# Kernel optimization log

Hardware: AMD Instinct MI355X
Metric: run time of the kernel (lower is better)

Reference implementation:

```python
import jax, jax.numpy as jnp
import numpy as np
from jax import lax

NB_VERTICES = 2048  # init kwarg nb_vertices
N_POINTS = 524288


def setup_inputs() -> dict:
    key = jax.random.key(0)
    pos = jax.random.normal(key, (N_POINTS, 3), dtype=jnp.float32)
    return {"pos": pos}


def _fps_indices(pos, m):
    """Single-pass iterative farthest point sampling.
    pos: [N, 3] float. Returns int32 indices [m].
    Maintains a running min squared-distance buffer (classic FPS).
    """
    N = pos.shape[0]
    big = jnp.asarray(jnp.finfo(pos.dtype).max, pos.dtype)
    min_d = jnp.full((N,), big, dtype=pos.dtype)
    idxs = jnp.zeros((m,), dtype=jnp.int32)  # idxs[0] = 0 (deterministic start)

    def body(i, carry):
        min_d, idxs = carry
        last = jnp.take(pos, idxs[i - 1], axis=0)          # [3]
        d = jnp.sum((pos - last[None, :]) ** 2, axis=-1)    # [N]
        min_d = jnp.minimum(min_d, d)
        nxt = jnp.argmax(min_d).astype(jnp.int32)
        idxs = idxs.at[i].set(nxt)
        return (min_d, idxs)

    _, idxs = lax.fori_loop(1, m, body, (min_d, idxs))
    return idxs


@jax.jit
def _forward(pos):
    # ratio = nb_vertices / N  ->  fps returns ceil(N*ratio) = nb_vertices
    # indices in a single pass, so the original while-loop runs once.
    idxs = _fps_indices(pos, NB_VERTICES)
    return pos[idxs]  # [nb_vertices, 3]


def reference(pos):
    return _forward(pos)
```

## Files before the change

### kernel.cpp

```cpp
#include <hip/hip_runtime.h>
#include <float.h>


#define NPTS     524288
#define MOUT     2048
#define NBLK     64
#define NTHR     512
#define NWAVE    (NTHR / 64)
#define GTHREADS (NBLK * NTHR)
#define PPT      (NPTS / GTHREADS)
#define SLOT_STRIDE 8
#define MASK51   ((1ull << 51) - 1)


__global__ void __launch_bounds__(NTHR, 1) fps_kernel(
    const float* __restrict__ pos, float* __restrict__ out,
    unsigned long long* __restrict__ slots)
{
    const unsigned tid = threadIdx.x;
    const unsigned blk = blockIdx.x;
    const unsigned g   = blk * NTHR + tid;

    float X[PPT], Y[PPT], Z[PPT], D[PPT];
#pragma unroll
    for (int p = 0; p < PPT; ++p) {
        const unsigned idx = g + (unsigned)p * GTHREADS;
        X[p] = pos[3u * idx + 0];
        Y[p] = pos[3u * idx + 1];
        Z[p] = pos[3u * idx + 2];
        D[p] = FLT_MAX;
    }

    float px = pos[0], py = pos[1], pz = pos[2];
    if (g == 0) { out[0] = px; out[1] = py; out[2] = pz; }

    __shared__ unsigned long long sred[NWAVE];
    __shared__ float sx, sy, sz;

    for (int i = 1; i < MOUT; ++i) {
        float bv = -1.0f;
        unsigned bi = 0;
#pragma unroll
        for (int p = 0; p < PPT; ++p) {
            float dx = __fsub_rn(X[p], px);
            float dy = __fsub_rn(Y[p], py);
            float dz = __fsub_rn(Z[p], pz);
            float d  = __fadd_rn(__fadd_rn(__fmul_rn(dx, dx), __fmul_rn(dy, dy)),
                                 __fmul_rn(dz, dz));
            float m  = fminf(D[p], d);
            D[p] = m;
            if (m > bv) { bv = m; bi = g + (unsigned)p * GTHREADS; }
        }
        unsigned long long best =
            ((unsigned long long)__float_as_uint(bv) << 19) |
            (unsigned long long)((NPTS - 1u) - bi);

#pragma unroll
        for (int off = 32; off > 0; off >>= 1) {
            unsigned long long o = __shfl_down(best, off, 64);
            if (o > best) best = o;
        }
        if ((tid & 63u) == 0u) sred[tid >> 6] = best;
        __syncthreads();

        if (tid < 64u) {
            unsigned long long b2 = (tid < NWAVE) ? sred[tid] : 0ull;
#pragma unroll
            for (int off = NWAVE / 2; off > 0; off >>= 1) {
                unsigned long long o = __shfl_down(b2, off, 64);
                if (o > b2) b2 = o;
            }
            unsigned long long* buf = slots + (unsigned)(i & 1) * (NBLK * SLOT_STRIDE);
            if (tid == 0u) {
                __hip_atomic_store(&buf[blk * SLOT_STRIDE],
                                   ((unsigned long long)i << 51) | b2,
                                   __ATOMIC_RELAXED, __HIP_MEMORY_SCOPE_AGENT);
            }
            const unsigned long long tag = (unsigned long long)i;
            unsigned long long s;
            do {
                s = __hip_atomic_load(&buf[tid * SLOT_STRIDE],
                                      __ATOMIC_RELAXED, __HIP_MEMORY_SCOPE_AGENT);
                if ((s >> 51) == tag) break;
                __builtin_amdgcn_s_sleep(1);
            } while (true);
            unsigned long long v = s & MASK51;
#pragma unroll
            for (int off = 32; off > 0; off >>= 1) {
                unsigned long long o = __shfl_down(v, off, 64);
                if (o > v) v = o;
            }
            if (tid == 0u) {
                unsigned widx = (NPTS - 1u) - (unsigned)(v & 0x7FFFFull);
                float x = pos[3u * widx + 0];
                float y = pos[3u * widx + 1];
                float z = pos[3u * widx + 2];
                sx = x; sy = y; sz = z;
                if (blk == 0) {
                    out[3 * i + 0] = x; out[3 * i + 1] = y; out[3 * i + 2] = z;
                }
            }
        }
        __syncthreads();
        px = sx; py = sy; pz = sz;
    }
}

extern "C" void kernel_launch(void* const* d_in, const int* in_sizes, int n_in,
                              void* d_out, int out_size, void* d_ws, size_t ws_size,
                              hipStream_t stream) {
    const float* pos = (const float*)d_in[0];
    float* out = (float*)d_out;
    unsigned long long* slots = (unsigned long long*)d_ws;

    void* args[] = { (void*)&pos, (void*)&out, (void*)&slots };
    hipLaunchCooperativeKernel((void*)fps_kernel, dim3(NBLK), dim3(NTHR),
                               args, 0, stream);
}
```

Before: 5.265 ms.

## Use single-wave blocks to drop intra-block barriers in FPS reduction

Changes the grid to 512 blocks of one 64-thread wave each. This removes the shared-memory stage and both __syncthreads per iteration. Each wave publishes its argmax to a global slot, then every wave polls all 512 slots itself, reduces them, and has each lane prefetch its own candidate's coordinates before the final shuffle reduction. The aim is to cut barrier and serial-lane latency on the critical path of each of the 2048 iterations. The cost is more global polling traffic per iteration, and a cooperative launch of 512 blocks must all be co-resident.

Result: slower. 9.101 ms (+72.8%).

```diff
diff --git a/kernel.cpp b/kernel.cpp
--- a/kernel.cpp
+++ b/kernel.cpp
@@ -4,12 +4,11 @@
 
 #define NPTS     524288
 #define MOUT     2048
-#define NBLK     64
-#define NTHR     512
-#define NWAVE    (NTHR / 64)
+#define NBLK     512
+#define NTHR     64
 #define GTHREADS (NBLK * NTHR)
 #define PPT      (NPTS / GTHREADS)
-#define SLOT_STRIDE 8
+#define KPL      (NBLK / 64)
 #define MASK51   ((1ull << 51) - 1)
 
 
@@ -17,9 +16,9 @@
     const float* __restrict__ pos, float* __restrict__ out,
     unsigned long long* __restrict__ slots)
 {
-    const unsigned tid = threadIdx.x;
-    const unsigned blk = blockIdx.x;
-    const unsigned g   = blk * NTHR + tid;
+    const unsigned lane = threadIdx.x;
+    const unsigned blk  = blockIdx.x;
+    const unsigned g    = blk * NTHR + lane;
 
     float X[PPT], Y[PPT], Z[PPT], D[PPT];
 #pragma unroll
@@ -33,9 +32,6 @@
 
     float px = pos[0], py = pos[1], pz = pos[2];
     if (g == 0) { out[0] = px; out[1] = py; out[2] = pz; }
-
-    __shared__ unsigned long long sred[NWAVE];
-    __shared__ float sx, sy, sz;
 
     for (int i = 1; i < MOUT; ++i) {
         float bv = -1.0f;
@@ -57,52 +53,56 @@
 
 #pragma unroll
         for (int off = 32; off > 0; off >>= 1) {
-            unsigned long long o = __shfl_down(best, off, 64);
+            unsigned long long o = __shfl_xor(best, off, 64);
             if (o > best) best = o;
         }
-        if ((tid & 63u) == 0u) sred[tid >> 6] = best;
-        __syncthreads();
 
-        if (tid < 64u) {
-            unsigned long long b2 = (tid < NWAVE) ? sred[tid] : 0ull;
+        unsigned long long* buf = slots + (unsigned)(i & 1) * NBLK;
+        if (lane == 0) {
+            __hip_atomic_store(&buf[blk], ((unsigned long long)i << 51) | best,
+                               __ATOMIC_RELAXED, __HIP_MEMORY_SCOPE_AGENT);
+        }
+
+        const unsigned long long tag = (unsigned long long)i;
+        unsigned long long v[KPL];
+        for (;;) {
+            bool ok = true;
 #pragma unroll
-            for (int off = NWAVE / 2; off > 0; off >>= 1) {
-                unsigned long long o = __shfl_down(b2, off, 64);
-                if (o > b2) b2 = o;
-            }
-            unsigned long long* buf = slots + (unsigned)(i & 1) * (NBLK * SLOT_STRIDE);
-            if (tid == 0u) {
-                __hip_atomic_store(&buf[blk * SLOT_STRIDE],
-                                   ((unsigned long long)i << 51) | b2,
-                                   __ATOMIC_RELAXED, __HIP_MEMORY_SCOPE_AGENT);
-            }
-            const unsigned long long tag = (unsigned long long)i;
-            unsigned long long s;
-            do {
-                s = __hip_atomic_load(&buf[tid * SLOT_STRIDE],
-                                      __ATOMIC_RELAXED, __HIP_MEMORY_SCOPE_AGENT);
-                if ((s >> 51) == tag) break;
-                __builtin_amdgcn_s_sleep(1);
-            } while (true);
-            unsigned long long v = s & MASK51;
+            for (int k = 0; k < KPL; ++k)
+                v[k] = __hip_atomic_load(&buf[lane + (unsigned)k * 64u],
+                                         __ATOMIC_RELAXED, __HIP_MEMORY_SCOPE_AGENT);
 #pragma unroll
-            for (int off = 32; off > 0; off >>= 1) {
-                unsigned long long o = __shfl_down(v, off, 64);
-                if (o > v) v = o;
-            }
-            if (tid == 0u) {
-                unsigned widx = (NPTS - 1u) - (unsigned)(v & 0x7FFFFull);
-                float x = pos[3u * widx + 0];
-                float y = pos[3u * widx + 1];
-                float z = pos[3u * widx + 2];
-                sx = x; sy = y; sz = z;
-                if (blk == 0) {
-                    out[3 * i + 0] = x; out[3 * i + 1] = y; out[3 * i + 2] = z;
-                }
-            }
+            for (int k = 0; k < KPL; ++k) ok &= ((v[k] >> 51) == tag);
+            if (__all(ok)) break;
+            __builtin_amdgcn_s_sleep(1);
         }
-        __syncthreads();
-        px = sx; py = sy; pz = sz;
+
+        unsigned long long c = v[0] & MASK51;
+#pragma unroll
+        for (int k = 1; k < KPL; ++k) {
+            unsigned long long w = v[k] & MASK51;
+            if (w > c) c = w;
+        }
+        unsigned cidx = (NPTS - 1u) - (unsigned)(c & 0x7FFFFull);
+        float cx = pos[3u * cidx + 0];
+        float cy = pos[3u * cidx + 1];
+        float cz = pos[3u * cidx + 2];
+
+        unsigned long long win = c;
+#pragma unroll
+        for (int off = 32; off > 0; off >>= 1) {
+            unsigned long long o = __shfl_xor(win, off, 64);
+            if (o > win) win = o;
+        }
+        unsigned long long bal = __ballot(win == c);
+        int src = __ffsll((unsigned long long)bal) - 1;
+        px = __shfl(cx, src, 64);
+        py = __shfl(cy, src, 64);
+        pz = __shfl(cz, src, 64);
+
+        if (blk == 0 && lane == 0) {
+            out[3 * i + 0] = px; out[3 * i + 1] = py; out[3 * i + 2] = pz;
+        }
     }
 }
 
```
